# Kernel tuning notes

Hardware: AMD Instinct MI355X
Metric: run time of the kernel (lower is better)

## Reference

```python
import jax, jax.numpy as jnp
import numpy as np
import math

B, S, E, H = 4, 2048, 1024, 16
D = E // H
INFINITY = 1000000.0

def setup_inputs() -> dict:
    key = jax.random.key(0)
    ks = jax.random.split(key, 10)
    std = 1.0 / math.sqrt(E)
    inp = {
        "x": jax.random.normal(ks[0], (B, S, E), dtype=jnp.float32),
        "mask": jax.random.randint(ks[1], (B, S), 0, 2).astype(jnp.bool_),
        "WQ_w": jax.random.uniform(ks[2], (E, E), jnp.float32, -std, std),
        "WQ_b": jax.random.uniform(ks[3], (E,), jnp.float32, -std, std),
        "WK_w": jax.random.uniform(ks[4], (E, E), jnp.float32, -std, std),
        "WK_b": jax.random.uniform(ks[5], (E,), jnp.float32, -std, std),
        "WV_w": jax.random.uniform(ks[6], (E, E), jnp.float32, -std, std),
        "WV_b": jax.random.uniform(ks[7], (E,), jnp.float32, -std, std),
        "WO_w": jax.random.uniform(ks[8], (E, E), jnp.float32, -std, std),
        "WO_b": jax.random.uniform(ks[9], (E,), jnp.float32, -std, std),
    }
    return inp

def reference(x, mask, WQ_w, WQ_b, WK_w, WK_b, WV_w, WV_b, WO_w, WO_b):
    # Linear layers: y = x @ W.T + b (torch convention)
    q = (x @ WQ_w.T + WQ_b).reshape(B, S, H, D).transpose(0, 2, 1, 3)  # (B,H,S,D)
    k = (x @ WK_w.T + WK_b).reshape(B, S, H, D).transpose(0, 2, 1, 3)
    v = (x @ WV_w.T + WV_b).reshape(B, S, H, D).transpose(0, 2, 1, 3)
    score = jnp.einsum("bhqd,bhkd->bhqk", q, k) / math.sqrt(D)  # (B,H,S,S)
    # additive key mask: -infinity where mask is False
    inv_mask = (~mask).astype(jnp.float32)[:, None, None, :]  # (B,1,1,S)
    score = score - inv_mask * INFINITY
    attn = jax.nn.softmax(score, axis=-1)
    o = jnp.einsum("bhqk,bhkd->bhqd", attn, v)  # (B,H,S,D)
    o = o.transpose(0, 2, 1, 3).reshape(B, S, E)
    o = o @ WO_w.T + WO_b
    o = jnp.abs(o * mask.astype(jnp.float32)[:, :, None])
    return o
```

## Files before the change

kernel.cpp:

```cpp
#include <hip/hip_runtime.h>
#include <math.h>

#define B_ 4
#define S_ 2048
#define E_ 1024
#define H_ 16
#define D_ 64
#define MTOT (B_*S_)

typedef _Float16 half8v __attribute__((ext_vector_type(8)));
typedef _Float16 half4v __attribute__((ext_vector_type(4)));
typedef float f32x4 __attribute__((ext_vector_type(4)));
typedef float f32x16 __attribute__((ext_vector_type(16)));
typedef unsigned uint4v __attribute__((ext_vector_type(4)));

typedef __attribute__((address_space(1))) const void gconst_void;
typedef __attribute__((address_space(3))) void lds_void;

#define MFMA16(a,b,c) __builtin_amdgcn_mfma_f32_16x16x32_f16((a),(b),(c),0,0,0)
#define MFMA32(a,b,c) __builtin_amdgcn_mfma_f32_32x32x16_f16((a),(b),(c),0,0,0)

#define QSCALE 0.18033688011112042f

static __device__ __forceinline__ unsigned cvt_pk_u32(float a, float b) {
  return __builtin_bit_cast(unsigned, __builtin_amdgcn_cvt_pkrtz(a, b));
}

#if __has_builtin(__builtin_amdgcn_permlane32_swap)
static __device__ __forceinline__ void pl32_swap(unsigned a, unsigned b,
                                                 unsigned& rlo, unsigned& rhi) {
  auto r = __builtin_amdgcn_permlane32_swap(a, b, false, false);
  rlo = r[0]; rhi = r[1];
}
#else
static __device__ __forceinline__ void pl32_swap(unsigned a, unsigned b,
                                                 unsigned& rlo, unsigned& rhi) {
  const int hi = (threadIdx.x & 63) >> 5;
  unsigned t = __shfl_xor(hi ? a : b, 32);
  rlo = hi ? t : a;
  rhi = hi ? b : t;
}
#endif

static __device__ __forceinline__ float partner32(float v, int hi) {
  unsigned u = __builtin_bit_cast(unsigned, v);
  unsigned lo_, hi_;
  pl32_swap(u, u, lo_, hi_);
  return __builtin_bit_cast(float, hi ? lo_ : hi_);
}

__global__ __launch_bounds__(256) void mask_prep_w(
    const unsigned char* __restrict__ mraw,
    _Float16* __restrict__ maskc, float* __restrict__ qmask,
    int* __restrict__ ks, int* __restrict__ nkpa,
    const float* __restrict__ w0, const float* __restrict__ w1,
    const float* __restrict__ w2, const float* __restrict__ w3,
    _Float16* __restrict__ o0, _Float16* __restrict__ o1,
    _Float16* __restrict__ o2, _Float16* __restrict__ o3) {
  const int gid = blockIdx.x;
  const int tid = threadIdx.x;
  if (gid >= 4) {
    const int rid = gid - 4;
    const int wsel = rid >> 10, blk = rid & 1023;
    const float* in = (wsel == 0) ? w0 : (wsel == 1) ? w1 : (wsel == 2) ? w2 : w3;
    _Float16* o = (wsel == 0) ? o0 : (wsel == 1) ? o1 : (wsel == 2) ? o2 : o3;
    const int i = (blk * 256 + tid) * 4;
    float4 v = *(const float4*)(in + i);
    half4v h;
    h[0] = (_Float16)v.x; h[1] = (_Float16)v.y; h[2] = (_Float16)v.z; h[3] = (_Float16)v.w;
    *(half4v*)(o + i) = h;
    return;
  }
  __shared__ int flags[2];
  __shared__ int psum[256];
  const int b = gid;
  if (tid < 2) flags[tid] = 1;
  __syncthreads();
  const unsigned int* w = (const unsigned int*)mraw;
  for (int i = tid; i < 2048; i += 256) {
    unsigned int v = w[i];
    if (!(v == 0u || v == 1u)) flags[0] = 0;
    if (!(v == 0u || v == 0x3f800000u)) flags[1] = 0;
  }
  __syncthreads();
  const int is_i32 = flags[0], is_f32 = flags[1];
  int m[8]; int cnt = 0;
  for (int i = 0; i < 8; ++i) {
    const int idx = b * 2048 + tid * 8 + i;
    int mv;
    if (is_i32)      mv = ((const int*)mraw)[idx];
    else if (is_f32) mv = (((const unsigned int*)mraw)[idx] != 0u);
    else             mv = (mraw[idx] != 0);
    m[i] = mv; cnt += mv;
    qmask[idx] = mv ? 1.0f : 0.0f;
  }
  psum[tid] = cnt;
  __syncthreads();
  for (int off = 1; off < 256; off <<= 1) {
    int u = (tid >= off) ? psum[tid - off] : 0;
    __syncthreads();
    psum[tid] += u;
    __syncthreads();
  }
  const int total = psum[255];
  int base = psum[tid] - cnt;
  for (int i = 0; i < 8; ++i)
    if (m[i]) ks[b * 2048 + (base++)] = tid * 8 + i;
  for (int j = tid; j < 2048; j += 256)
    maskc[b * 2048 + j] = (j < total) ? (_Float16)0.0f : (_Float16)(-60000.0f);
  __syncthreads();
  const int lastv = (total > 0) ? ks[b * 2048 + total - 1] : 0;
  for (int j = total + tid; j < 2048; j += 256)
    ks[b * 2048 + j] = lastv;
  if (tid == 0) nkpa[b] = (total + 127) & ~127;
}

__global__ __launch_bounds__(256) void prep_fused(
    const float* __restrict__ x, const int* __restrict__ ks,
    const int* __restrict__ nkpa, _Float16* __restrict__ xc,
    const float* __restrict__ qmask, float* __restrict__ out) {
  const int id = blockIdx.x;
  if (id < 8192) {
    const int j = id & 2047, b = id >> 11;
    if (j >= nkpa[b]) return;
    const int s = ks[b * 2048 + j];
    const float* src = x + (size_t)(b * 2048 + s) * E_;
    _Float16* dst = xc + (size_t)(b * 2048 + j) * E_;
    const int i = threadIdx.x * 4;
    float4 v = *(const float4*)(src + i);
    half4v h;
    h[0] = (_Float16)v.x; h[1] = (_Float16)v.y; h[2] = (_Float16)v.z; h[3] = (_Float16)v.w;
    *(half4v*)(dst + i) = h;
  } else {
    const int row = id - 8192;
    if (qmask[row] != 0.0f) return;
    float4 z = make_float4(0.f, 0.f, 0.f, 0.f);
    *(float4*)(out + (size_t)row * E_ + threadIdx.x * 4) = z;
  }
}

template <int ROWS>
__device__ __forceinline__ void stageX64s(const _Float16* __restrict__ g, int ld,
                                          _Float16* lds, int wid, int lane) {
#pragma unroll
  for (int j = 0; j < ROWS / 32; ++j) {
    const int c = j * 256 + wid * 64 + lane;
    const int row = c >> 3, dslot = c & 7;
    const int sslot = dslot ^ (row & 7);
    const _Float16* src = g + (size_t)row * ld + sslot * 8;
    _Float16* dst = lds + (size_t)(j * 256 + wid * 64) * 8;
    __builtin_amdgcn_global_load_lds((gconst_void*)src, (lds_void*)dst, 16, 0, 0);
  }
}

__device__ __forceinline__ void stage256x64w(const _Float16* __restrict__ g, int ld,
                                             _Float16* lds, int wid, int lane) {
#pragma unroll
  for (int j = 0; j < 4; ++j) {
    const int c = j * 512 + wid * 64 + lane;
    const int row = c >> 3, dslot = c & 7;
    const int sslot = dslot ^ (row & 7);
    const _Float16* src = g + (size_t)row * ld + sslot * 8;
    _Float16* dst = lds + (size_t)(j * 512 + wid * 64) * 8;
    __builtin_amdgcn_global_load_lds((gconst_void*)src, (lds_void*)dst, 16, 0, 0);
  }
}

__global__ __launch_bounds__(512) void qkv_gemm(
    const _Float16* __restrict__ xc, const int* __restrict__ nkpa,
    const _Float16* __restrict__ wq, const _Float16* __restrict__ wk, const _Float16* __restrict__ wv,
    const float* __restrict__ bq, const float* __restrict__ bkp, const float* __restrict__ bvp,
    _Float16* __restrict__ Qc, _Float16* __restrict__ Kc, _Float16* __restrict__ Vc) {
  const int id = blockIdx.x;
  const int tt = id / 48;
  const int r = id % 48;
  const int bb = r / 12;
  const int r2 = r % 12;
  const int by = r2 / 3, z = r2 % 3;
  if (tt * 256 >= nkpa[bb]) return;
  __shared__ _Float16 As[2][256 * 64];
  __shared__ _Float16 Bs[2][256 * 64];
  const int tid = threadIdx.x, lane = tid & 63, wid = tid >> 6;
  const int g = lane >> 4, r16 = lane & 15;
  const int wr = wid >> 2, wc = wid & 3;
  const int sw = r16 & 7;
  const int bm = bb * 2048 + tt * 256, bn = by * 256;
  const _Float16* w = (z == 0) ? wq : (z == 1) ? wk : wv;
  const float* bias = (z == 0) ? bq : (z == 1) ? bkp : bvp;
  f32x4 acc[8][4] = {};
  stage256x64w(xc + (size_t)bm * E_, E_, As[0], wid, lane);
  stage256x64w(w + (size_t)bn * E_, E_, Bs[0], wid, lane);
  __syncthreads();
  int cur = 0;
  for (int k0 = 0; k0 < E_; k0 += 64) {
    const int kn = k0 + 64;
    if (kn < E_) {
      stage256x64w(xc + (size_t)bm * E_ + kn, E_, As[cur ^ 1], wid, lane);
      stage256x64w(w + (size_t)bn * E_ + kn, E_, Bs[cur ^ 1], wid, lane);
    }
    const _Float16* Ac = As[cur];
    const _Float16* Bc = Bs[cur];
#pragma unroll
    for (int kk = 0; kk < 2; ++kk) {
      const int so = ((kk * 4 + g) ^ sw) * 8;
      half8v a[8], bf[4];
#pragma unroll
      for (int i = 0; i < 8; ++i) a[i] = *(const half8v*)&Ac[(wr * 128 + i * 16 + r16) * 64 + so];
#pragma unroll
      for (int j = 0; j < 4; ++j) bf[j] = *(const half8v*)&Bc[(wc * 64 + j * 16 + r16) * 64 + so];
      __builtin_amdgcn_s_setprio(1);
#pragma unroll
      for (int i = 0; i < 8; ++i)
#pragma unroll
        for (int j = 0; j < 4; ++j) acc[i][j] = MFMA16(a[i], bf[j], acc[i][j]);
      __builtin_amdgcn_s_setprio(0);
    }
    __syncthreads();
    cur ^= 1;
  }
#pragma unroll
  for (int i = 0; i < 8; ++i) {
#pragma unroll
    for (int j = 0; j < 4; ++j) {
      const int gn = bn + wc * 64 + j * 16 + r16;
      const float bb2 = bias[gn];
      const int h = gn >> 6, d = gn & 63;
      const int gm0 = bm + wr * 128 + i * 16 + g * 4;
      const int b_ = gm0 >> 11, s0 = gm0 & (S_ - 1);
      const size_t bhbase = (size_t)(b_ * H_ + h) * S_ * D_;
      if (z == 2) {
        half4v v4;
#pragma unroll
        for (int ii = 0; ii < 4; ++ii) v4[ii] = (_Float16)(acc[i][j][ii] + bb2);
        *(half4v*)&Vc[bhbase + (size_t)(s0 >> 4) * (D_ * 16) + d * 16 + (s0 & 15)] = v4;
      } else if (z == 1) {
#pragma unroll
        for (int ii = 0; ii < 4; ++ii) {
          const int s = s0 + ii;
          Kc[bhbase + (size_t)(s >> 5) * 2048 + (d >> 4) * 512 + (s & 31) * 16 + (d & 15)] =
              (_Float16)(acc[i][j][ii] + bb2);
        }
      } else {
#pragma unroll
        for (int ii = 0; ii < 4; ++ii)
          Qc[bhbase + (size_t)(s0 + ii) * D_ + d] = (_Float16)((acc[i][j][ii] + bb2) * QSCALE);
      }
    }
  }
}

__global__ __launch_bounds__(512) void attn_kernel(
    const _Float16* __restrict__ Qc, const _Float16* __restrict__ Kc, const _Float16* __restrict__ Vc,
    const _Float16* __restrict__ maskc, const int* __restrict__ nkpa,
    _Float16* __restrict__ Oc) {
  __shared__ float mlds[2][2][64][36];
  _Float16* smask = (_Float16*)&mlds[0][0][0][0];
  const int tid = threadIdx.x, lane = tid & 63, wid = tid >> 6;
  const int c = lane & 31, hi = lane >> 5;
  const int qg = wid & 1, kh = wid >> 1;
  const int id = blockIdx.x;
  const int slot = id & 7, hbh = (id >> 3) & 7, t = id >> 6;
  const int hb = hbh * 8 + slot;
  const int b = hb >> 4, h = hb & 15;
  const int nkp = nkpa[b];
  if (t * 64 >= nkp) return;
  const size_t bh = (size_t)(b * H_ + h);
  const _Float16* Qb = Qc + bh * S_ * D_;
  const _Float16* Kb = Kc + bh * S_ * D_;
  const _Float16* Vb = Vc + bh * S_ * D_;

  *((half4v*)smask + tid) = *((const half4v*)(maskc + (size_t)b * S_) + tid);

  const int jq = t * 64 + qg * 32 + c;

  half8v qb[4];
#pragma unroll
  for (int kc = 0; kc < 4; ++kc)
    qb[kc] = *(const half8v*)&Qb[(size_t)jq * D_ + 16 * kc + 8 * hi];

  half8v bone = {};
  if (hi == 0) bone[0] = (_Float16)1.0f;
  const f32x16 fzero = {};

  f32x16 oacc[2] = {};
  float mrun = -1e30f, lrun = 0.f;
  const int laneoff = c * 16 + 8 * hi;
  const int nkq = nkp >> 2;
  const int kb0 = kh * nkq;

  __syncthreads();

  half8v kaf[4];
  {
    const _Float16* ktb = Kb + (size_t)(kb0 >> 5) * 2048 + laneoff;
#pragma unroll
    for (int kc = 0; kc < 4; ++kc) kaf[kc] = *(const half8v*)&ktb[kc * 512];
  }
  _Float16 mv = smask[kb0 + c];

  for (int kb = kb0; kb < kb0 + nkq; kb += 32) {
    half8v amask = {};
    if (hi == 0) amask[0] = mv;
    __builtin_amdgcn_s_setprio(1);
    f32x16 sc = MFMA32(amask, bone, fzero);
    sc = MFMA32(kaf[0], qb[0], sc);
    sc = MFMA32(kaf[1], qb[1], sc);
    sc = MFMA32(kaf[2], qb[2], sc);
    sc = MFMA32(kaf[3], qb[3], sc);
    __builtin_amdgcn_s_setprio(0);
    const int kbn = (kb + 32 < kb0 + nkq) ? kb + 32 : kb0;
    {
      const _Float16* ktb = Kb + (size_t)(kbn >> 5) * 2048 + laneoff;
#pragma unroll
      for (int kc = 0; kc < 4; ++kc) kaf[kc] = *(const half8v*)&ktb[kc * 512];
    }
    mv = smask[kbn + c];
    const _Float16* v_base = Vb + (size_t)(kb >> 4) * (D_ * 16) + laneoff;
    half8v va00 = *(const half8v*)&v_base[0];
    half8v va01 = *(const half8v*)&v_base[512];
    half8v va10 = *(const half8v*)&v_base[1024];
    half8v va11 = *(const half8v*)&v_base[1024 + 512];
    float t0 = fmaxf(sc[0], sc[4]), t1 = fmaxf(sc[1], sc[5]);
    float t2 = fmaxf(sc[2], sc[6]), t3 = fmaxf(sc[3], sc[7]);
    t0 = fmaxf(fmaxf(sc[8], sc[12]), t0);
    t1 = fmaxf(fmaxf(sc[9], sc[13]), t1);
    t2 = fmaxf(fmaxf(sc[10], sc[14]), t2);
    t3 = fmaxf(fmaxf(sc[11], sc[15]), t3);
    float pmax = fmaxf(fmaxf(t0, t1), fmaxf(t2, t3));
    pmax = fmaxf(pmax, partner32(pmax, hi));
    if (__any(pmax > mrun + 11.0f)) {
      float mnew = fmaxf(mrun, pmax);
      float corr = __builtin_amdgcn_exp2f(mrun - mnew);
      mrun = mnew;
      lrun *= corr;
#pragma unroll
      for (int dt = 0; dt < 2; ++dt)
#pragma unroll
        for (int r = 0; r < 16; ++r) oacc[dt][r] *= corr;
    }
    float ps0 = 0.f, ps1 = 0.f;
#pragma unroll
    for (int sl = 0; sl < 2; ++sl) {
      const int bs = 8 * sl;
      float p0 = __builtin_amdgcn_exp2f(sc[bs + 0] - mrun);
      float p1 = __builtin_amdgcn_exp2f(sc[bs + 1] - mrun);
      float p2 = __builtin_amdgcn_exp2f(sc[bs + 2] - mrun);
      float p3 = __builtin_amdgcn_exp2f(sc[bs + 3] - mrun);
      float p4 = __builtin_amdgcn_exp2f(sc[bs + 4] - mrun);
      float p5 = __builtin_amdgcn_exp2f(sc[bs + 5] - mrun);
      float p6 = __builtin_amdgcn_exp2f(sc[bs + 6] - mrun);
      float p7 = __builtin_amdgcn_exp2f(sc[bs + 7] - mrun);
      ps0 += (p0 + p1) + (p2 + p3);
      ps1 += (p4 + p5) + (p6 + p7);
      unsigned uA = cvt_pk_u32(p0, p1);
      unsigned uB = cvt_pk_u32(p2, p3);
      unsigned uC = cvt_pk_u32(p4, p5);
      unsigned uD = cvt_pk_u32(p6, p7);
      unsigned w0, w1, w2, w3;
      pl32_swap(uA, uC, w0, w2);
      pl32_swap(uB, uD, w1, w3);
      uint4v u4 = {w0, w1, w2, w3};
      half8v pb = __builtin_bit_cast(half8v, u4);
      __builtin_amdgcn_s_setprio(1);
      oacc[0] = MFMA32(sl ? va10 : va00, pb, oacc[0]);
      oacc[1] = MFMA32(sl ? va11 : va01, pb, oacc[1]);
      __builtin_amdgcn_s_setprio(0);
    }
    lrun += ps0 + ps1;
  }
  lrun += partner32(lrun, hi);
  __syncthreads();
  if (kh >= 2) {
    float* p = &mlds[qg][kh - 2][lane][0];
#pragma unroll
    for (int dt = 0; dt < 2; ++dt)
#pragma unroll
      for (int rr = 0; rr < 4; ++rr) {
        float4 v4 = make_float4(oacc[dt][4 * rr], oacc[dt][4 * rr + 1],
                                oacc[dt][4 * rr + 2], oacc[dt][4 * rr + 3]);
        *(float4*)&p[dt * 16 + rr * 4] = v4;
      }
    p[32] = mrun;
    p[33] = lrun;
  }
  __syncthreads();
  if (kh < 2) {
    const float* p = &mlds[qg][kh][lane][0];
    const float mB = p[32], lB = p[33];
    const float mS = fmaxf(mrun, mB);
    const float cA = __builtin_amdgcn_exp2f(mrun - mS);
    const float cB = __builtin_amdgcn_exp2f(mB - mS);
#pragma unroll
    for (int dt = 0; dt < 2; ++dt)
#pragma unroll
      for (int rr = 0; rr < 4; ++rr) {
        float4 vB = *(const float4*)&p[dt * 16 + rr * 4];
        oacc[dt][4 * rr + 0] = oacc[dt][4 * rr + 0] * cA + vB.x * cB;
        oacc[dt][4 * rr + 1] = oacc[dt][4 * rr + 1] * cA + vB.y * cB;
        oacc[dt][4 * rr + 2] = oacc[dt][4 * rr + 2] * cA + vB.z * cB;
        oacc[dt][4 * rr + 3] = oacc[dt][4 * rr + 3] * cA + vB.w * cB;
      }
    lrun = lrun * cA + lB * cB;
    mrun = mS;
  }
  __syncthreads();
  if (kh == 1) {
    float* p = &mlds[qg][0][lane][0];
#pragma unroll
    for (int dt = 0; dt < 2; ++dt)
#pragma unroll
      for (int rr = 0; rr < 4; ++rr) {
        float4 v4 = make_float4(oacc[dt][4 * rr], oacc[dt][4 * rr + 1],
                                oacc[dt][4 * rr + 2], oacc[dt][4 * rr + 3]);
        *(float4*)&p[dt * 16 + rr * 4] = v4;
      }
    p[32] = mrun;
    p[33] = lrun;
  }
  __syncthreads();
  if (kh == 0) {
    const float* p = &mlds[qg][0][lane][0];
    const float mB = p[32], lB = p[33];
    const float mS = fmaxf(mrun, mB);
    const float cA = __builtin_amdgcn_exp2f(mrun - mS);
    const float cB = __builtin_amdgcn_exp2f(mB - mS);
    const float inv = 1.0f / (lrun * cA + lB * cB);
    const float fA = cA * inv, fB = cB * inv;
    _Float16* orow = Oc + ((size_t)(b * S_ + jq)) * E_ + h * D_;
#pragma unroll
    for (int dt = 0; dt < 2; ++dt)
#pragma unroll
      for (int rr = 0; rr < 4; ++rr) {
        float4 vB = *(const float4*)&p[dt * 16 + rr * 4];
        half4v o4;
        o4[0] = (_Float16)(oacc[dt][4 * rr + 0] * fA + vB.x * fB);
        o4[1] = (_Float16)(oacc[dt][4 * rr + 1] * fA + vB.y * fB);
        o4[2] = (_Float16)(oacc[dt][4 * rr + 2] * fA + vB.z * fB);
        o4[3] = (_Float16)(oacc[dt][4 * rr + 3] * fA + vB.w * fB);
        *(half4v*)&orow[32 * dt + 8 * rr + 4 * hi] = o4;
      }
  }
}

__global__ __launch_bounds__(256) void oproj_gemm(
    const _Float16* __restrict__ Oc, const _Float16* __restrict__ wo, const float* __restrict__ bo,
    const int* __restrict__ ks, const int* __restrict__ nkpa, float* __restrict__ out) {
  const int id = blockIdx.x;
  const int jt = id / 32;
  const int rem = id % 32;
  const int bb = rem / 8, by = rem % 8;
  if (jt * 64 >= nkpa[bb]) return;
  __shared__ _Float16 As[2][64 * 64];
  __shared__ _Float16 Bs[2][128 * 64];
  const int tid = threadIdx.x, lane = tid & 63, wid = tid >> 6;
  const int g = lane >> 4, r16 = lane & 15;
  const int bm = bb * 2048 + jt * 64, bn = by * 128;
  const int wr = wid >> 1, wc = wid & 1;
  const int sw = r16 & 7;
  f32x4 acc[2][4] = {};
  stageX64s<64>(Oc + (size_t)bm * E_, E_, As[0], wid, lane);
  stageX64s<128>(wo + (size_t)bn * E_, E_, Bs[0], wid, lane);
  __syncthreads();
  int cur = 0;
  for (int k0 = 0; k0 < E_; k0 += 64) {
    const int kn = k0 + 64;
    if (kn < E_) {
      stageX64s<64>(Oc + (size_t)bm * E_ + kn, E_, As[cur ^ 1], wid, lane);
      stageX64s<128>(wo + (size_t)bn * E_ + kn, E_, Bs[cur ^ 1], wid, lane);
    }
    const _Float16* Ac = As[cur];
    const _Float16* Bc = Bs[cur];
#pragma unroll
    for (int kk = 0; kk < 2; ++kk) {
      const int so = ((kk * 4 + g) ^ sw) * 8;
      half8v a[2], bf[4];
#pragma unroll
      for (int i = 0; i < 2; ++i) a[i] = *(const half8v*)&Ac[(wr * 32 + i * 16 + r16) * 64 + so];
#pragma unroll
      for (int j = 0; j < 4; ++j) bf[j] = *(const half8v*)&Bc[(wc * 64 + j * 16 + r16) * 64 + so];
#pragma unroll
      for (int i = 0; i < 2; ++i)
#pragma unroll
        for (int j = 0; j < 4; ++j) acc[i][j] = MFMA16(a[i], bf[j], acc[i][j]);
    }
    __syncthreads();
    cur ^= 1;
  }
#pragma unroll
  for (int i = 0; i < 2; ++i) {
#pragma unroll
    for (int j = 0; j < 4; ++j) {
      const int gn = bn + wc * 64 + j * 16 + r16;
      const float bb2 = bo[gn];
      const int gm0 = bm + wr * 32 + i * 16 + g * 4;
#pragma unroll
      for (int ii = 0; ii < 4; ++ii) {
        const int gm = gm0 + ii;
        const int b_ = gm >> 11, j_ = gm & (S_ - 1);
        const int sorig = ks[b_ * 2048 + j_];
        const float y = acc[i][j][ii] + bb2;
        out[((size_t)(b_ * S_ + sorig)) * E_ + gn] = fabsf(y);
      }
    }
  }
}

extern "C" void kernel_launch(void* const* d_in, const int* in_sizes, int n_in,
                              void* d_out, int out_size, void* d_ws, size_t ws_size,
                              hipStream_t stream) {
  const float* x = (const float*)d_in[0];
  const unsigned char* mask = (const unsigned char*)d_in[1];
  const float* WQ_w = (const float*)d_in[2];
  const float* WQ_b = (const float*)d_in[3];
  const float* WK_w = (const float*)d_in[4];
  const float* WK_b = (const float*)d_in[5];
  const float* WV_w = (const float*)d_in[6];
  const float* WV_b = (const float*)d_in[7];
  const float* WO_w = (const float*)d_in[8];
  const float* WO_b = (const float*)d_in[9];

  char* ws = (char*)d_ws;
  size_t off = 0;
  _Float16* xc  = (_Float16*)(ws + off); off += (size_t)MTOT * E_ * 2;
  _Float16* wqh = (_Float16*)(ws + off); off += (size_t)E_ * E_ * 2;
  _Float16* wkh = (_Float16*)(ws + off); off += (size_t)E_ * E_ * 2;
  _Float16* wvh = (_Float16*)(ws + off); off += (size_t)E_ * E_ * 2;
  _Float16* woh = (_Float16*)(ws + off); off += (size_t)E_ * E_ * 2;
  _Float16* Qc  = (_Float16*)(ws + off); off += (size_t)MTOT * E_ * 2;
  _Float16* Kc  = (_Float16*)(ws + off); off += (size_t)MTOT * E_ * 2;
  _Float16* Vc  = (_Float16*)(ws + off); off += (size_t)MTOT * E_ * 2;
  _Float16* Oc  = (_Float16*)(ws + off); off += (size_t)MTOT * E_ * 2;
  _Float16* maskcf = (_Float16*)(ws + off); off += (size_t)B_ * S_ * 2;
  float* qmaskf = (float*)(ws + off); off += (size_t)B_ * S_ * 4;
  int* ksl      = (int*)(ws + off); off += (size_t)B_ * S_ * 4;
  int* nkpa     = (int*)(ws + off); off += 64;
  if (ws_size < off) return;

  mask_prep_w<<<dim3(4100), dim3(256), 0, stream>>>(
      mask, maskcf, qmaskf, ksl, nkpa,
      WQ_w, WK_w, WV_w, WO_w, wqh, wkh, wvh, woh);
  prep_fused<<<dim3(16384), dim3(256), 0, stream>>>(
      x, ksl, nkpa, xc, qmaskf, (float*)d_out);
  qkv_gemm<<<dim3(384), dim3(512), 0, stream>>>(
      xc, nkpa, wqh, wkh, wvh, WQ_b, WK_b, WV_b, Qc, Kc, Vc);
  attn_kernel<<<dim3((S_ / 64) * H_ * B_), dim3(512), 0, stream>>>(
      Qc, Kc, Vc, maskcf, nkpa, Oc);
  oproj_gemm<<<dim3(32 * 32), dim3(256), 0, stream>>>(Oc, woh, WO_b, ksl, nkpa, (float*)d_out);
}
```

Measured before the change: 125.5 us.

## Retile QKV GEMM to 256x128 with triple-buffered LDS pipeline

Halves the QKV GEMM N-tile to 128, doubling the grid to 768 blocks, and replaces the double-buffered loop with a three-slot ring. Loads run two k-steps ahead, using explicit vmcnt waits and raw barriers instead of __syncthreads. Fragments are read into registers before the next prefetch is issued. Padding of the compacted key count is raised to a multiple of 256 so it matches the M-tile. The intent is more parallelism and better load/MFMA overlap, at the cost of more A-tile reloads, and the larger padding adds some wasted work in later stages.

```diff
diff --git a/kernel.cpp b/kernel.cpp
--- a/kernel.cpp
+++ b/kernel.cpp
@@ -112,7 +112,7 @@
   const int lastv = (total > 0) ? ks[b * 2048 + total - 1] : 0;
   for (int j = total + tid; j < 2048; j += 256)
     ks[b * 2048 + j] = lastv;
-  if (tid == 0) nkpa[b] = (total + 127) & ~127;
+  if (tid == 0) nkpa[b] = (total + 255) & ~255;
 }
 
 __global__ __launch_bounds__(256) void prep_fused(
@@ -153,14 +153,26 @@
   }
 }
 
-__device__ __forceinline__ void stage256x64w(const _Float16* __restrict__ g, int ld,
-                                             _Float16* lds, int wid, int lane) {
+__device__ __forceinline__ void stageA256(const _Float16* __restrict__ g,
+                                          _Float16* lds, int wid, int lane) {
 #pragma unroll
   for (int j = 0; j < 4; ++j) {
     const int c = j * 512 + wid * 64 + lane;
     const int row = c >> 3, dslot = c & 7;
     const int sslot = dslot ^ (row & 7);
-    const _Float16* src = g + (size_t)row * ld + sslot * 8;
+    const _Float16* src = g + (size_t)row * E_ + sslot * 8;
+    _Float16* dst = lds + (size_t)(j * 512 + wid * 64) * 8;
+    __builtin_amdgcn_global_load_lds((gconst_void*)src, (lds_void*)dst, 16, 0, 0);
+  }
+}
+__device__ __forceinline__ void stageB128(const _Float16* __restrict__ g,
+                                          _Float16* lds, int wid, int lane) {
+#pragma unroll
+  for (int j = 0; j < 2; ++j) {
+    const int c = j * 512 + wid * 64 + lane;
+    const int row = c >> 3, dslot = c & 7;
+    const int sslot = dslot ^ (row & 7);
+    const _Float16* src = g + (size_t)row * E_ + sslot * 8;
     _Float16* dst = lds + (size_t)(j * 512 + wid * 64) * 8;
     __builtin_amdgcn_global_load_lds((gconst_void*)src, (lds_void*)dst, 16, 0, 0);
   }
@@ -172,60 +184,71 @@
     const float* __restrict__ bq, const float* __restrict__ bkp, const float* __restrict__ bvp,
     _Float16* __restrict__ Qc, _Float16* __restrict__ Kc, _Float16* __restrict__ Vc) {
   const int id = blockIdx.x;
-  const int tt = id / 48;
-  const int r = id % 48;
-  const int bb = r / 12;
-  const int r2 = r % 12;
-  const int by = r2 / 3, z = r2 % 3;
-  if (tt * 256 >= nkpa[bb]) return;
-  __shared__ _Float16 As[2][256 * 64];
-  __shared__ _Float16 Bs[2][256 * 64];
+  const int tt = id / 24;
+  const int rem = id % 24;
+  const int by = rem / 3, z = rem % 3;
+  const int bb = tt >> 3, mtile = tt & 7;
+  if (mtile * 256 >= nkpa[bb]) return;
+  __shared__ _Float16 Asr[3 * 256 * 64];
+  __shared__ _Float16 Bsr[3 * 128 * 64];
   const int tid = threadIdx.x, lane = tid & 63, wid = tid >> 6;
   const int g = lane >> 4, r16 = lane & 15;
-  const int wr = wid >> 2, wc = wid & 3;
+  const int wr = wid >> 1, wc = wid & 1;
   const int sw = r16 & 7;
-  const int bm = bb * 2048 + tt * 256, bn = by * 256;
+  const int bm = bb * 2048 + mtile * 256, bn = by * 128;
   const _Float16* w = (z == 0) ? wq : (z == 1) ? wk : wv;
   const float* bias = (z == 0) ? bq : (z == 1) ? bkp : bvp;
-  f32x4 acc[8][4] = {};
-  stage256x64w(xc + (size_t)bm * E_, E_, As[0], wid, lane);
-  stage256x64w(w + (size_t)bn * E_, E_, Bs[0], wid, lane);
-  __syncthreads();
-  int cur = 0;
-  for (int k0 = 0; k0 < E_; k0 += 64) {
-    const int kn = k0 + 64;
-    if (kn < E_) {
-      stage256x64w(xc + (size_t)bm * E_ + kn, E_, As[cur ^ 1], wid, lane);
-      stage256x64w(w + (size_t)bn * E_ + kn, E_, Bs[cur ^ 1], wid, lane);
-    }
-    const _Float16* Ac = As[cur];
-    const _Float16* Bc = Bs[cur];
+  const _Float16* Abase = xc + (size_t)bm * E_;
+  const _Float16* Bbase = w + (size_t)bn * E_;
+  f32x4 acc[4][4] = {};
+  stageA256(Abase + 0, Asr, wid, lane);
+  stageB128(Bbase + 0, Bsr, wid, lane);
+  stageA256(Abase + 64, Asr + 256 * 64, wid, lane);
+  stageB128(Bbase + 64, Bsr + 128 * 64, wid, lane);
+  asm volatile("s_waitcnt vmcnt(6)" ::: "memory");
+  __builtin_amdgcn_s_barrier();
+  for (int t = 0; t < 16; ++t) {
+    const int slot = t % 3;
+    const _Float16* Ac = Asr + slot * (256 * 64);
+    const _Float16* Bc = Bsr + slot * (128 * 64);
+    half8v a[2][4], bfr[2][4];
 #pragma unroll
     for (int kk = 0; kk < 2; ++kk) {
       const int so = ((kk * 4 + g) ^ sw) * 8;
-      half8v a[8], bf[4];
-#pragma unroll
-      for (int i = 0; i < 8; ++i) a[i] = *(const half8v*)&Ac[(wr * 128 + i * 16 + r16) * 64 + so];
-#pragma unroll
-      for (int j = 0; j < 4; ++j) bf[j] = *(const half8v*)&Bc[(wc * 64 + j * 16 + r16) * 64 + so];
-      __builtin_amdgcn_s_setprio(1);
-#pragma unroll
-      for (int i = 0; i < 8; ++i)
-#pragma unroll
-        for (int j = 0; j < 4; ++j) acc[i][j] = MFMA16(a[i], bf[j], acc[i][j]);
-      __builtin_amdgcn_s_setprio(0);
-    }
-    __syncthreads();
-    cur ^= 1;
-  }
-#pragma unroll
-  for (int i = 0; i < 8; ++i) {
+#pragma unroll
+      for (int i = 0; i < 4; ++i)
+        a[kk][i] = *(const half8v*)&Ac[(wr * 64 + i * 16 + r16) * 64 + so];
+#pragma unroll
+      for (int j = 0; j < 4; ++j)
+        bfr[kk][j] = *(const half8v*)&Bc[(wc * 64 + j * 16 + r16) * 64 + so];
+    }
+    if (t < 14) {
+      const int s2 = (t + 2) % 3;
+      stageA256(Abase + (size_t)(t + 2) * 64, Asr + s2 * (256 * 64), wid, lane);
+      stageB128(Bbase + (size_t)(t + 2) * 64, Bsr + s2 * (128 * 64), wid, lane);
+      asm volatile("s_waitcnt vmcnt(6)" ::: "memory");
+    } else if (t == 14) {
+      asm volatile("s_waitcnt vmcnt(0)" ::: "memory");
+    }
+    __builtin_amdgcn_s_setprio(1);
+#pragma unroll
+    for (int kk = 0; kk < 2; ++kk)
+#pragma unroll
+      for (int i = 0; i < 4; ++i)
+#pragma unroll
+        for (int j = 0; j < 4; ++j)
+          acc[i][j] = MFMA16(a[kk][i], bfr[kk][j], acc[i][j]);
+    __builtin_amdgcn_s_setprio(0);
+    __builtin_amdgcn_s_barrier();
+  }
+#pragma unroll
+  for (int i = 0; i < 4; ++i) {
 #pragma unroll
     for (int j = 0; j < 4; ++j) {
       const int gn = bn + wc * 64 + j * 16 + r16;
       const float bb2 = bias[gn];
       const int h = gn >> 6, d = gn & 63;
-      const int gm0 = bm + wr * 128 + i * 16 + g * 4;
+      const int gm0 = bm + wr * 64 + i * 16 + g * 4;
       const int b_ = gm0 >> 11, s0 = gm0 & (S_ - 1);
       const size_t bhbase = (size_t)(b_ * H_ + h) * S_ * D_;
       if (z == 2) {
@@ -541,7 +564,7 @@
       WQ_w, WK_w, WV_w, WO_w, wqh, wkh, wvh, woh);
   prep_fused<<<dim3(16384), dim3(256), 0, stream>>>(
       x, ksl, nkpa, xc, qmaskf, (float*)d_out);
-  qkv_gemm<<<dim3(384), dim3(512), 0, stream>>>(
+  qkv_gemm<<<dim3(768), dim3(512), 0, stream>>>(
       xc, nkpa, wqh, wkh, wvh, WQ_b, WK_b, WV_b, Qc, Kc, Vc);
   attn_kernel<<<dim3((S_ / 64) * H_ * B_), dim3(512), 0, stream>>>(
       Qc, Kc, Vc, maskcf, nkpa, Oc);
```

Result: slower. 128.2 us (+2.2%).
